# Performance work log

Hardware: AMD Instinct MI355X
Metric: run time of the kernel (lower is better)

The kernel has to match this reference:

```python
import jax, jax.numpy as jnp
import numpy as np


def setup_inputs() -> dict:
    key = jax.random.key(0)
    k1, k2 = jax.random.split(key)
    B, T, S, D = 8, 1024, 1024, 2048
    support_sets = jax.random.normal(k1, (B, S, D), dtype=jnp.float32)
    X_hats = jax.random.normal(k2, (B, T, D), dtype=jnp.float32)
    return {"support_sets": support_sets, "X_hats": X_hats}


def reference(support_sets, X_hats):
    # Pairwise cosine similarity: out[b, t, s] = cos(X_hats[b, t], support_sets[b, s])
    # Matches torch.nn.functional.cosine_similarity with eps=1e-10:
    #   dot / max(||x|| * ||y||, eps)
    eps = 1e-10
    x_norm = jnp.linalg.norm(X_hats, axis=-1)          # [B, T]
    s_norm = jnp.linalg.norm(support_sets, axis=-1)    # [B, S]
    dots = jnp.einsum('btd,bsd->bts', X_hats, support_sets)  # [B, T, S]
    denom = jnp.maximum(x_norm[:, :, None] * s_norm[:, None, :], eps)
    return dots / denom
```

## Files before the change

kernel.cpp:

```cpp
#include <hip/hip_runtime.h>
#include <hip/hip_bf16.h>

typedef __attribute__((ext_vector_type(4))) float        f32x4;
typedef __attribute__((ext_vector_type(8))) short        s16x8;
typedef __attribute__((ext_vector_type(4))) unsigned int u32x4;

#define Bb 8
#define Tt 1024
#define Ss 1024
#define Dd 2048
#define BM 128
#define BN 128
#define BK 32
#define LDK 40

__device__ __forceinline__ unsigned pack2_bf16(float f0, float f1) {
  unsigned u0 = __builtin_bit_cast(unsigned, f0) + 0x8000u;
  unsigned u1 = __builtin_bit_cast(unsigned, f1) + 0x8000u;
  return (u0 >> 16) | (u1 & 0xffff0000u);
}

__global__ __launch_bounds__(256, 2)
void paircos_kernel(const float* __restrict__ sup,
                    const float* __restrict__ xh,
                    float* __restrict__ out)
{
  __shared__ short As[BM * LDK];
  __shared__ short Bs[BN * LDK];
  __shared__ float invA[BM];
  __shared__ float invB[BN];

  const int bid  = blockIdx.x;
  const int b    = bid >> 6;
  const int tile = bid & 63;
  const int tm   = tile >> 3;
  const int tn   = tile & 7;

  const float* Abase = xh  + (size_t)(b * Tt + tm * BM) * Dd;
  const float* Bbase = sup + (size_t)(b * Ss + tn * BN) * Dd;

  const int t   = threadIdx.x;
  const int row = t >> 1;
  const int kh  = t & 1;

  const f32x4* agp = (const f32x4*)(Abase + (size_t)row * Dd + kh * 16);
  const f32x4* bgp = (const f32x4*)(Bbase + (size_t)row * Dd + kh * 16);

  u32x4* awr = (u32x4*)(As + row * LDK + kh * 16);
  u32x4* bwr = (u32x4*)(Bs + row * LDK + kh * 16);

  const int wave = t >> 6;
  const int lane = t & 63;
  const int wm   = (wave >> 1) << 6;
  const int wn   = (wave & 1) << 6;
  const int lm   = lane & 15;
  const int kq   = lane >> 4;

  f32x4 acc[4][4];
  #pragma unroll
  for (int i = 0; i < 4; ++i)
    #pragma unroll
    for (int j = 0; j < 4; ++j)
      acc[i][j] = (f32x4)0.0f;

  float sqa = 0.0f, sqb = 0.0f;

  f32x4 areg[4], breg[4];
  #pragma unroll
  for (int i = 0; i < 4; ++i) { areg[i] = agp[i]; breg[i] = bgp[i]; }

  for (int k0 = 0; k0 < Dd; k0 += BK) {
    unsigned pa[8], pb[8];
    #pragma unroll
    for (int i = 0; i < 4; ++i) {
      sqa = fmaf(areg[i][0], areg[i][0], sqa);
      sqa = fmaf(areg[i][1], areg[i][1], sqa);
      sqa = fmaf(areg[i][2], areg[i][2], sqa);
      sqa = fmaf(areg[i][3], areg[i][3], sqa);
      pa[i * 2 + 0] = pack2_bf16(areg[i][0], areg[i][1]);
      pa[i * 2 + 1] = pack2_bf16(areg[i][2], areg[i][3]);
      sqb = fmaf(breg[i][0], breg[i][0], sqb);
      sqb = fmaf(breg[i][1], breg[i][1], sqb);
      sqb = fmaf(breg[i][2], breg[i][2], sqb);
      sqb = fmaf(breg[i][3], breg[i][3], sqb);
      pb[i * 2 + 0] = pack2_bf16(breg[i][0], breg[i][1]);
      pb[i * 2 + 1] = pack2_bf16(breg[i][2], breg[i][3]);
    }

    __syncthreads();
    awr[0] = (u32x4){pa[0], pa[1], pa[2], pa[3]};
    awr[1] = (u32x4){pa[4], pa[5], pa[6], pa[7]};
    bwr[0] = (u32x4){pb[0], pb[1], pb[2], pb[3]};
    bwr[1] = (u32x4){pb[4], pb[5], pb[6], pb[7]};
    __syncthreads();

    if (k0 + BK < Dd) {
      const int off = (k0 + BK) >> 2;
      #pragma unroll
      for (int i = 0; i < 4; ++i) { areg[i] = agp[off + i]; breg[i] = bgp[off + i]; }
    }

    s16x8 af[4], bfr[4];
    #pragma unroll
    for (int i = 0; i < 4; ++i) {
      af[i]  = *(const s16x8*)(As + (wm + i * 16 + lm) * LDK + kq * 8);
      bfr[i] = *(const s16x8*)(Bs + (wn + i * 16 + lm) * LDK + kq * 8);
    }
    #pragma unroll
    for (int mi = 0; mi < 4; ++mi)
      #pragma unroll
      for (int ni = 0; ni < 4; ++ni)
        acc[mi][ni] = __builtin_amdgcn_mfma_f32_16x16x32_bf16(af[mi], bfr[ni], acc[mi][ni], 0, 0, 0);
  }

  __syncthreads();
  ((float*)As)[t] = sqa;
  ((float*)Bs)[t] = sqb;
  __syncthreads();
  if (t < 128) {
    invA[t] = 1.0f / sqrtf(((float*)As)[2 * t] + ((float*)As)[2 * t + 1]);
    invB[t] = 1.0f / sqrtf(((float*)Bs)[2 * t] + ((float*)Bs)[2 * t + 1]);
  }
  __syncthreads();

  float* outb = out + (size_t)(b * Tt + tm * BM) * Ss + tn * BN;
  const int m0 = wm + kq * 4;
  const int n0 = wn + lm;
  #pragma unroll
  for (int mi = 0; mi < 4; ++mi) {
    #pragma unroll
    for (int r = 0; r < 4; ++r) {
      const int mrow = m0 + mi * 16 + r;
      const float ia = invA[mrow];
      float* orow = outb + (size_t)mrow * Ss;
      #pragma unroll
      for (int ni = 0; ni < 4; ++ni) {
        const int ncol = n0 + ni * 16;
        orow[ncol] = acc[mi][ni][r] * (ia * invB[ncol]);
      }
    }
  }
}

extern "C" void kernel_launch(void* const* d_in, const int* in_sizes, int n_in,
                              void* d_out, int out_size, void* d_ws, size_t ws_size,
                              hipStream_t stream) {
  const float* sup = (const float*)d_in[0];
  const float* xh  = (const float*)d_in[1];
  float* out = (float*)d_out;
  dim3 grid(Bb * (Tt / BM) * (Ss / BN));
  paircos_kernel<<<grid, dim3(256), 0, stream>>>(sup, xh, out);
}
```

Before: 233.4 us.

## Pre-convert inputs to bf16 with norms, then GEMM via direct global-to-LDS loads

Adds a pre-pass kernel that converts both fp32 inputs to bf16 in the workspace and computes inverse row norms. The GEMM then streams half-width bf16 tiles straight into LDS with global_load_lds, using an XOR-swizzled unpadded layout in place of the padded one. The aim is to stop every output tile from re-reading fp32 data and re-converting it, at the cost of an extra kernel launch and a full bf16 copy written to and read back from memory. The old fused kernel stays as a fallback when the workspace is too small.

```diff
diff --git a/kernel.cpp b/kernel.cpp
--- a/kernel.cpp
+++ b/kernel.cpp
@@ -4,6 +4,7 @@
 typedef __attribute__((ext_vector_type(4))) float        f32x4;
 typedef __attribute__((ext_vector_type(8))) short        s16x8;
 typedef __attribute__((ext_vector_type(4))) unsigned int u32x4;
+typedef __attribute__((ext_vector_type(2))) unsigned int u32x2;
 
 #define Bb 8
 #define Tt 1024
@@ -12,7 +13,6 @@
 #define BM 128
 #define BN 128
 #define BK 32
-#define LDK 40
 
 __device__ __forceinline__ unsigned pack2_bf16(float f0, float f1) {
   unsigned u0 = __builtin_bit_cast(unsigned, f0) + 0x8000u;
@@ -20,15 +20,44 @@
   return (u0 >> 16) | (u1 & 0xffff0000u);
 }
 
+__device__ __forceinline__ void gld_lds16(const void* g, void* l) {
+  __builtin_amdgcn_global_load_lds(
+      (__attribute__((address_space(1))) void*)(void*)(g),
+      (__attribute__((address_space(3))) void*)l, 16, 0, 0);
+}
+
+__global__ __launch_bounds__(256, 4)
+void convert_kernel(const float* __restrict__ sup, const float* __restrict__ xh,
+                    unsigned* __restrict__ abf, unsigned* __restrict__ bbf,
+                    float* __restrict__ invA, float* __restrict__ invB)
+{
+  const int wave = threadIdx.x >> 6, lane = threadIdx.x & 63;
+  const int rowg = blockIdx.x * 4 + wave;
+  const float* src; unsigned* dst; float* inv; int row;
+  if (rowg < 8192) { row = rowg;         src = xh;  dst = abf; inv = invA; }
+  else             { row = rowg - 8192;  src = sup; dst = bbf; inv = invB; }
+
+  const f32x4* s4 = (const f32x4*)(src + (size_t)row * Dd);
+  u32x2* d2 = (u32x2*)(dst + (size_t)row * (Dd / 2));
+  float sq = 0.0f;
+  #pragma unroll
+  for (int j = 0; j < 8; ++j) {
+    f32x4 v = s4[j * 64 + lane];
+    sq = fmaf(v[0], v[0], fmaf(v[1], v[1], fmaf(v[2], v[2], fmaf(v[3], v[3], sq))));
+    d2[j * 64 + lane] = (u32x2){pack2_bf16(v[0], v[1]), pack2_bf16(v[2], v[3])};
+  }
+  #pragma unroll
+  for (int m = 32; m; m >>= 1) sq += __shfl_xor(sq, m, 64);
+  if (lane == 0) inv[row] = 1.0f / sqrtf(sq);
+}
+
 __global__ __launch_bounds__(256, 2)
-void paircos_kernel(const float* __restrict__ sup,
-                    const float* __restrict__ xh,
-                    float* __restrict__ out)
+void gemm_kernel(const short* __restrict__ abf, const short* __restrict__ bbf,
+                 const float* __restrict__ invA, const float* __restrict__ invB,
+                 float* __restrict__ out)
 {
-  __shared__ short As[BM * LDK];
-  __shared__ short Bs[BN * LDK];
-  __shared__ float invA[BM];
-  __shared__ float invB[BN];
+  __shared__ short As[BM * BK];
+  __shared__ short Bs[BN * BK];
 
   const int bid  = blockIdx.x;
   const int b    = bid >> 6;
@@ -36,25 +65,29 @@
   const int tm   = tile >> 3;
   const int tn   = tile & 7;
 
-  const float* Abase = xh  + (size_t)(b * Tt + tm * BM) * Dd;
-  const float* Bbase = sup + (size_t)(b * Ss + tn * BN) * Dd;
-
-  const int t   = threadIdx.x;
-  const int row = t >> 1;
-  const int kh  = t & 1;
-
-  const f32x4* agp = (const f32x4*)(Abase + (size_t)row * Dd + kh * 16);
-  const f32x4* bgp = (const f32x4*)(Bbase + (size_t)row * Dd + kh * 16);
-
-  u32x4* awr = (u32x4*)(As + row * LDK + kh * 16);
-  u32x4* bwr = (u32x4*)(Bs + row * LDK + kh * 16);
-
-  const int wave = t >> 6;
-  const int lane = t & 63;
-  const int wm   = (wave >> 1) << 6;
-  const int wn   = (wave & 1) << 6;
-  const int lm   = lane & 15;
-  const int kq   = lane >> 4;
+  const int t = threadIdx.x, wave = t >> 6, lane = t & 63;
+
+  const int srow  = lane >> 2;
+  const int cphys = lane & 3;
+  const int r0    = wave * 32;
+  const int rA0 = r0 + srow, rA1 = r0 + 16 + srow;
+  const int cl0 = cphys ^ ((rA0 >> 1) & 3);
+  const int cl1 = cphys ^ ((rA1 >> 1) & 3);
+
+  const short* ga0 = abf + (size_t)(b * Tt + tm * BM + rA0) * Dd + cl0 * 8;
+  const short* ga1 = abf + (size_t)(b * Tt + tm * BM + rA1) * Dd + cl1 * 8;
+  const short* gb0 = bbf + (size_t)(b * Ss + tn * BN + rA0) * Dd + cl0 * 8;
+  const short* gb1 = bbf + (size_t)(b * Ss + tn * BN + rA1) * Dd + cl1 * 8;
+  short* lA0 = As + r0 * BK;
+  short* lA1 = As + (r0 + 16) * BK;
+  short* lB0 = Bs + r0 * BK;
+  short* lB1 = Bs + (r0 + 16) * BK;
+
+  const int wm = (wave >> 1) << 6;
+  const int wn = (wave & 1) << 6;
+  const int lm = lane & 15;
+  const int kq = lane >> 4;
+  const int swk = (kq ^ ((lm >> 1) & 3)) * 8;
 
   f32x4 acc[4][4];
   #pragma unroll
@@ -63,48 +96,20 @@
     for (int j = 0; j < 4; ++j)
       acc[i][j] = (f32x4)0.0f;
 
-  float sqa = 0.0f, sqb = 0.0f;
-
-  f32x4 areg[4], breg[4];
-  #pragma unroll
-  for (int i = 0; i < 4; ++i) { areg[i] = agp[i]; breg[i] = bgp[i]; }
-
   for (int k0 = 0; k0 < Dd; k0 += BK) {
-    unsigned pa[8], pb[8];
+    __syncthreads();
+    gld_lds16(ga0, lA0);
+    gld_lds16(ga1, lA1);
+    gld_lds16(gb0, lB0);
+    gld_lds16(gb1, lB1);
+    ga0 += BK; ga1 += BK; gb0 += BK; gb1 += BK;
+    __syncthreads();
+
+    s16x8 af[4], bfr[4];
     #pragma unroll
     for (int i = 0; i < 4; ++i) {
-      sqa = fmaf(areg[i][0], areg[i][0], sqa);
-      sqa = fmaf(areg[i][1], areg[i][1], sqa);
-      sqa = fmaf(areg[i][2], areg[i][2], sqa);
-      sqa = fmaf(areg[i][3], areg[i][3], sqa);
-      pa[i * 2 + 0] = pack2_bf16(areg[i][0], areg[i][1]);
-      pa[i * 2 + 1] = pack2_bf16(areg[i][2], areg[i][3]);
-      sqb = fmaf(breg[i][0], breg[i][0], sqb);
-      sqb = fmaf(breg[i][1], breg[i][1], sqb);
-      sqb = fmaf(breg[i][2], breg[i][2], sqb);
-      sqb = fmaf(breg[i][3], breg[i][3], sqb);
-      pb[i * 2 + 0] = pack2_bf16(breg[i][0], breg[i][1]);
-      pb[i * 2 + 1] = pack2_bf16(breg[i][2], breg[i][3]);
-    }
-
-    __syncthreads();
-    awr[0] = (u32x4){pa[0], pa[1], pa[2], pa[3]};
-    awr[1] = (u32x4){pa[4], pa[5], pa[6], pa[7]};
-    bwr[0] = (u32x4){pb[0], pb[1], pb[2], pb[3]};
-    bwr[1] = (u32x4){pb[4], pb[5], pb[6], pb[7]};
-    __syncthreads();
-
-    if (k0 + BK < Dd) {
-      const int off = (k0 + BK) >> 2;
-      #pragma unroll
-      for (int i = 0; i < 4; ++i) { areg[i] = agp[off + i]; breg[i] = bgp[off + i]; }
-    }
-
-    s16x8 af[4], bfr[4];
-    #pragma unroll
-    for (int i = 0; i < 4; ++i) {
-      af[i]  = *(const s16x8*)(As + (wm + i * 16 + lm) * LDK + kq * 8);
-      bfr[i] = *(const s16x8*)(Bs + (wn + i * 16 + lm) * LDK + kq * 8);
+      af[i]  = *(const s16x8*)(As + (wm + i * 16 + lm) * BK + swk);
+      bfr[i] = *(const s16x8*)(Bs + (wn + i * 16 + lm) * BK + swk);
     }
     #pragma unroll
     for (int mi = 0; mi < 4; ++mi)
@@ -113,19 +118,102 @@
         acc[mi][ni] = __builtin_amdgcn_mfma_f32_16x16x32_bf16(af[mi], bfr[ni], acc[mi][ni], 0, 0, 0);
   }
 
-  __syncthreads();
-  ((float*)As)[t] = sqa;
-  ((float*)Bs)[t] = sqb;
-  __syncthreads();
-  if (t < 128) {
-    invA[t] = 1.0f / sqrtf(((float*)As)[2 * t] + ((float*)As)[2 * t + 1]);
-    invB[t] = 1.0f / sqrtf(((float*)Bs)[2 * t] + ((float*)Bs)[2 * t + 1]);
-  }
-  __syncthreads();
-
+  const float* iA = invA + b * Tt + tm * BM;
+  const float* iB = invB + b * Ss + tn * BN;
   float* outb = out + (size_t)(b * Tt + tm * BM) * Ss + tn * BN;
   const int m0 = wm + kq * 4;
   const int n0 = wn + lm;
+  #pragma unroll
+  for (int mi = 0; mi < 4; ++mi) {
+    #pragma unroll
+    for (int r = 0; r < 4; ++r) {
+      const int mrow = m0 + mi * 16 + r;
+      const float ia = iA[mrow];
+      float* orow = outb + (size_t)mrow * Ss;
+      #pragma unroll
+      for (int ni = 0; ni < 4; ++ni) {
+        const int ncol = n0 + ni * 16;
+        orow[ncol] = acc[mi][ni][r] * (ia * iB[ncol]);
+      }
+    }
+  }
+}
+
+#define LDKF 40
+__global__ __launch_bounds__(256, 2)
+void paircos_kernel(const float* __restrict__ sup, const float* __restrict__ xh,
+                    float* __restrict__ out)
+{
+  __shared__ short As[BM * LDKF];
+  __shared__ short Bs[BN * LDKF];
+  __shared__ float invA[BM];
+  __shared__ float invB[BN];
+
+  const int bid = blockIdx.x;
+  const int b = bid >> 6, tile = bid & 63, tm = tile >> 3, tn = tile & 7;
+  const float* Abase = xh  + (size_t)(b * Tt + tm * BM) * Dd;
+  const float* Bbase = sup + (size_t)(b * Ss + tn * BN) * Dd;
+  const int t = threadIdx.x, row = t >> 1, kh = t & 1;
+  const f32x4* agp = (const f32x4*)(Abase + (size_t)row * Dd + kh * 16);
+  const f32x4* bgp = (const f32x4*)(Bbase + (size_t)row * Dd + kh * 16);
+  u32x4* awr = (u32x4*)(As + row * LDKF + kh * 16);
+  u32x4* bwr = (u32x4*)(Bs + row * LDKF + kh * 16);
+  const int wave = t >> 6, lane = t & 63;
+  const int wm = (wave >> 1) << 6, wn = (wave & 1) << 6;
+  const int lm = lane & 15, kq = lane >> 4;
+
+  f32x4 acc[4][4];
+  #pragma unroll
+  for (int i = 0; i < 4; ++i)
+    #pragma unroll
+    for (int j = 0; j < 4; ++j) acc[i][j] = (f32x4)0.0f;
+  float sqa = 0.0f, sqb = 0.0f;
+  f32x4 areg[4], breg[4];
+  #pragma unroll
+  for (int i = 0; i < 4; ++i) { areg[i] = agp[i]; breg[i] = bgp[i]; }
+
+  for (int k0 = 0; k0 < Dd; k0 += BK) {
+    unsigned pa[8], pb[8];
+    #pragma unroll
+    for (int i = 0; i < 4; ++i) {
+      sqa = fmaf(areg[i][0], areg[i][0], sqa); sqa = fmaf(areg[i][1], areg[i][1], sqa);
+      sqa = fmaf(areg[i][2], areg[i][2], sqa); sqa = fmaf(areg[i][3], areg[i][3], sqa);
+      pa[i*2+0] = pack2_bf16(areg[i][0], areg[i][1]); pa[i*2+1] = pack2_bf16(areg[i][2], areg[i][3]);
+      sqb = fmaf(breg[i][0], breg[i][0], sqb); sqb = fmaf(breg[i][1], breg[i][1], sqb);
+      sqb = fmaf(breg[i][2], breg[i][2], sqb); sqb = fmaf(breg[i][3], breg[i][3], sqb);
+      pb[i*2+0] = pack2_bf16(breg[i][0], breg[i][1]); pb[i*2+1] = pack2_bf16(breg[i][2], breg[i][3]);
+    }
+    __syncthreads();
+    awr[0] = (u32x4){pa[0],pa[1],pa[2],pa[3]}; awr[1] = (u32x4){pa[4],pa[5],pa[6],pa[7]};
+    bwr[0] = (u32x4){pb[0],pb[1],pb[2],pb[3]}; bwr[1] = (u32x4){pb[4],pb[5],pb[6],pb[7]};
+    __syncthreads();
+    if (k0 + BK < Dd) {
+      const int off = (k0 + BK) >> 2;
+      #pragma unroll
+      for (int i = 0; i < 4; ++i) { areg[i] = agp[off + i]; breg[i] = bgp[off + i]; }
+    }
+    s16x8 af[4], bfr[4];
+    #pragma unroll
+    for (int i = 0; i < 4; ++i) {
+      af[i]  = *(const s16x8*)(As + (wm + i*16 + lm) * LDKF + kq * 8);
+      bfr[i] = *(const s16x8*)(Bs + (wn + i*16 + lm) * LDKF + kq * 8);
+    }
+    #pragma unroll
+    for (int mi = 0; mi < 4; ++mi)
+      #pragma unroll
+      for (int ni = 0; ni < 4; ++ni)
+        acc[mi][ni] = __builtin_amdgcn_mfma_f32_16x16x32_bf16(af[mi], bfr[ni], acc[mi][ni], 0, 0, 0);
+  }
+  __syncthreads();
+  ((float*)As)[t] = sqa; ((float*)Bs)[t] = sqb;
+  __syncthreads();
+  if (t < 128) {
+    invA[t] = 1.0f / sqrtf(((float*)As)[2*t] + ((float*)As)[2*t+1]);
+    invB[t] = 1.0f / sqrtf(((float*)Bs)[2*t] + ((float*)Bs)[2*t+1]);
+  }
+  __syncthreads();
+  float* outb = out + (size_t)(b * Tt + tm * BM) * Ss + tn * BN;
+  const int m0 = wm + kq * 4, n0 = wn + lm;
   #pragma unroll
   for (int mi = 0; mi < 4; ++mi) {
     #pragma unroll
@@ -148,6 +236,20 @@
   const float* sup = (const float*)d_in[0];
   const float* xh  = (const float*)d_in[1];
   float* out = (float*)d_out;
-  dim3 grid(Bb * (Tt / BM) * (Ss / BN));
-  paircos_kernel<<<grid, dim3(256), 0, stream>>>(sup, xh, out);
-}
+
+  const size_t nElem = (size_t)Bb * Tt * Dd;
+  const size_t bfBytes = nElem * sizeof(short);
+  const size_t NEED = 2 * bfBytes + 2 * (size_t)Bb * Tt * sizeof(float);
+
+  if (ws_size >= NEED) {
+    unsigned* abf = (unsigned*)d_ws;
+    unsigned* bbf = (unsigned*)((char*)d_ws + bfBytes);
+    float* invA = (float*)((char*)d_ws + 2 * bfBytes);
+    float* invB = invA + (size_t)Bb * Tt;
+    convert_kernel<<<dim3(4096), dim3(256), 0, stream>>>(sup, xh, abf, bbf, invA, invB);
+    gemm_kernel<<<dim3(512), dim3(256), 0, stream>>>((const short*)abf, (const short*)bbf,
+                                                     invA, invB, out);
+  } else {
+    paircos_kernel<<<dim3(512), dim3(256), 0, stream>>>(sup, xh, out);
+  }
+}
```

New measurement: 210.0 us. 1.11x faster.
